# Kernel tuning notes

Hardware: AMD Instinct MI355X
Metric: run time of the kernel (lower is better)

The kernel has to match this reference:

```python
import jax, jax.numpy as jnp
import numpy as np

B, T, S = 2, 1024, 1024
D, H, L = 512, 8, 4
E, K, FF = 8, 2, 2048
V, BLK = 32000, 2048
DH = D // H
EPS = 1e-5


def setup_inputs() -> dict:
    key = jax.random.key(0)
    ks = jax.random.split(key, 20)
    n = lambda k, shp: jax.random.normal(k, shp, dtype=jnp.float32) * 0.02
    return {
        "decoder_input_ids": jax.random.randint(ks[0], (B, T), 0, V, dtype=jnp.int32),
        "enc_out": jax.random.normal(ks[1], (B, S, D), dtype=jnp.float32),
        "attention_mask": jnp.ones((B, T), dtype=jnp.int32),
        "embed_table": n(ks[2], (V, D)),
        "pos_table": n(ks[3], (BLK, D)),
        "sa_w": n(ks[4], (L, 4, D, D)),   # q,k,v,o projections for self-attn
        "sa_b": jnp.zeros((L, 4, D), jnp.float32),
        "ca_w": n(ks[5], (L, 4, D, D)),   # q,k,v,o projections for cross-attn
        "ca_b": jnp.zeros((L, 4, D), jnp.float32),
        "ln_g": jnp.ones((L, 3, D), jnp.float32),
        "ln_b": jnp.zeros((L, 3, D), jnp.float32),
        "router_w": n(ks[6], (L, D, E)),
        "router_b": jnp.zeros((L, E), jnp.float32),
        "exp_w1": n(ks[7], (L, E, D, FF)),
        "exp_b1": jnp.zeros((L, E, FF), jnp.float32),
        "exp_w2": n(ks[8], (L, E, FF, D)),
        "exp_b2": jnp.zeros((L, E, D), jnp.float32),
    }


def _layer_norm(x, g, b):
    mu = jnp.mean(x, axis=-1, keepdims=True)
    var = jnp.mean(jnp.square(x - mu), axis=-1, keepdims=True)
    return (x - mu) * jax.lax.rsqrt(var + EPS) * g + b


def _mha(q_in, kv_in, w, b, mask):
    # w: [4, D, D]; 0=q,1=k,2=v,3=out
    def split_heads(t):
        Bn, Tn, _ = t.shape
        return t.reshape(Bn, Tn, H, DH).transpose(0, 2, 1, 3)  # [B,H,T,dh]
    q = split_heads(q_in @ w[0] + b[0])
    k = split_heads(kv_in @ w[1] + b[1])
    v = split_heads(kv_in @ w[2] + b[2])
    scores = jnp.einsum("bhqd,bhkd->bhqk", q, k) / jnp.sqrt(jnp.float32(DH))
    if mask is not None:
        scores = jnp.where(mask, scores, jnp.float32(-1e9))
    attn = jax.nn.softmax(scores, axis=-1)
    out = jnp.einsum("bhqk,bhkd->bhqd", attn, v)
    out = out.transpose(0, 2, 1, 3).reshape(q_in.shape[0], q_in.shape[1], D)
    return out @ w[3] + b[3]


def _sparse_moe(x, rw, rb, w1, b1, w2, b2):
    # Router: softmax over experts, keep top-k, renormalize kept weights.
    logits = x @ rw + rb                       # [B,T,E]
    probs = jax.nn.softmax(logits, axis=-1)
    topv, topi = jax.lax.top_k(probs, K)       # [B,T,K]
    kmask = jnp.sum(jax.nn.one_hot(topi, E, dtype=x.dtype), axis=-2)  # [B,T,E]
    gates = probs * kmask
    gates = gates / jnp.sum(gates, axis=-1, keepdims=True)
    # Dense expert compute (faithful math, vectorized over experts).
    h = jax.nn.relu(jnp.einsum("btd,edf->btef", x, w1) + b1)   # [B,T,E,FF]
    eo = jnp.einsum("btef,efd->bted", h, w2) + b2              # [B,T,E,D]
    out = jnp.einsum("bte,bted->btd", gates, eo)
    # Load-balancing aux loss: E * sum_e f_e * P_e
    f = jnp.mean(kmask, axis=(0, 1))
    p = jnp.mean(probs, axis=(0, 1))
    lb = jnp.float32(E) * jnp.sum(f * p)
    return out, lb


def reference(decoder_input_ids, enc_out, attention_mask, embed_table, pos_table,
              sa_w, sa_b, ca_w, ca_b, ln_g, ln_b, router_w, router_b,
              exp_w1, exp_b1, exp_w2, exp_b2):
    Bn, Tn = decoder_input_ids.shape
    y = embed_table[decoder_input_ids] + pos_table[:Tn]  # [B,T,D]
    causal = jnp.tril(jnp.ones((Tn, Tn), dtype=bool))
    am = attention_mask.astype(bool)[:, None, None, :]   # [B,1,1,T]
    mask = causal[None, None] & am                       # [B,1,T,T]
    lb_total = jnp.float32(0.0)
    for i in range(L):
        sa = _mha(y, y, sa_w[i], sa_b[i], mask)
        y = _layer_norm(y + sa, ln_g[i, 0], ln_b[i, 0])
        ca = _mha(y, enc_out, ca_w[i], ca_b[i], None)
        y = _layer_norm(y + ca, ln_g[i, 1], ln_b[i, 1])
        mo, lb = _sparse_moe(y, router_w[i], router_b[i], exp_w1[i], exp_b1[i], exp_w2[i], exp_b2[i])
        lb_total = lb_total + lb
        y = _layer_norm(y + mo, ln_g[i, 2], ln_b[i, 2])
    return y, lb_total
```

## Files before the change

### kernel.cpp

```cpp
#include <hip/hip_runtime.h>
#include <math.h>

#define Bb 2
#define Tt 1024
#define Ss 1024
#define Dd 512
#define Hh 8
#define Ll 4
#define Ee 8
#define FFf 2048
#define Mm 2048
#define NPp 4096
#define EPSF 1e-5f
#define DD_ (Dd*Dd)
#define LOSC 1024.0f
#define ILOSC (1.0f/1024.0f)
#define RBLK 64
#define IMm (1.0f/(float)Mm)

typedef _Float16 f16;
typedef __attribute__((ext_vector_type(8))) _Float16 f16x8;
typedef __attribute__((ext_vector_type(4))) _Float16 f16x4;
typedef __attribute__((ext_vector_type(4))) float f32x4;

__device__ __forceinline__ void fsplit(float x, f16& h, f16& l) {
  h = (f16)x;
  l = (f16)((x - (float)h) * LOSC);
}

__device__ __forceinline__ void load16(const void* g, void* l) {
  __builtin_amdgcn_global_load_lds(
      (const __attribute__((address_space(1))) void*)g,
      (__attribute__((address_space(3))) void*)l, 16, 0, 0);
}

__global__ void embed_kernel(const int* __restrict__ ids,
                             const float* __restrict__ emb,
                             const float* __restrict__ pos,
                             float* __restrict__ Y,
                             f16* __restrict__ Yh, f16* __restrict__ Yl) {
  int m = blockIdx.x;
  int t = m % Tt;
  int id = ids[m];
  for (int d = threadIdx.x; d < Dd; d += 256) {
    float v = emb[(size_t)id * Dd + d] + pos[(size_t)t * Dd + d];
    Y[(size_t)m * Dd + d] = v;
    f16 h, l; fsplit(v, h, l);
    Yh[(size_t)m * Dd + d] = h;
    Yl[(size_t)m * Dd + d] = l;
  }
}

__global__ void cvt_split_kernel(const float* __restrict__ src,
                                 f16* __restrict__ dh, f16* __restrict__ dl) {
  size_t i = ((size_t)blockIdx.x * 256 + threadIdx.x) * 4;
  float4 v = *reinterpret_cast<const float4*>(&src[i]);
  float a[4] = {v.x, v.y, v.z, v.w};
#pragma unroll
  for (int j = 0; j < 4; j++) { f16 h, l; fsplit(a[j], h, l); dh[i + j] = h; dl[i + j] = l; }
}

__global__ void zero_kernel(float* __restrict__ p) {
  size_t i = ((size_t)blockIdx.x * 256 + threadIdx.x) * 4;
  *reinterpret_cast<float4*>(&p[i]) = make_float4(0.f, 0.f, 0.f, 0.f);
}

__global__ __launch_bounds__(256)
void transpose_split(const float* __restrict__ src,
                     f16* __restrict__ dstH, f16* __restrict__ dstL,
                     int Kd, int Nd) {
  __shared__ float Tl[32][33];
  size_t zo = (size_t)blockIdx.z * Kd * Nd;
  int k0 = blockIdx.y * 32, n0 = blockIdx.x * 32;
  int t = threadIdx.x;
  int r = t >> 3, c = t & 7;
  float4 v = *reinterpret_cast<const float4*>(&src[zo + (size_t)(k0 + r) * Nd + n0 + c * 4]);
  Tl[r][c * 4 + 0] = v.x; Tl[r][c * 4 + 1] = v.y;
  Tl[r][c * 4 + 2] = v.z; Tl[r][c * 4 + 3] = v.w;
  __syncthreads();
  int nl = t >> 3, kq = t & 7;
  f16x4 hv, lv;
#pragma unroll
  for (int i = 0; i < 4; i++) {
    f16 h, l; fsplit(Tl[kq * 4 + i][nl], h, l);
    hv[i] = h; lv[i] = l;
  }
  size_t o = zo + (size_t)(n0 + nl) * Kd + k0 + kq * 4;
  *reinterpret_cast<f16x4*>(&dstH[o]) = hv;
  *reinterpret_cast<f16x4*>(&dstL[o]) = lv;
}

template <bool GATHER, bool OSPLIT, bool RELU, bool GATE, int KS>
__global__ __launch_bounds__(256)
void mm128(const f16* __restrict__ Ah_, const f16* __restrict__ Al_, int lda,
           const f16* __restrict__ Bh_, const f16* __restrict__ Bl_,
           const float* __restrict__ bias,
           float* __restrict__ Cf, f16* __restrict__ Ch, f16* __restrict__ Cl, int ldc,
           int Mtot, int N, int K,
           const int* __restrict__ tok, const float* __restrict__ gate,
           const int* __restrict__ offs, const int* __restrict__ cnt) {
  __shared__ f16 Ash[128 * 32];
  __shared__ f16 Asl[128 * 32];
  __shared__ f16 Bsh[128 * 32];
  __shared__ f16 Bsl[128 * 32];
  int zz = blockIdx.z;
  int e  = (KS > 1) ? (zz / KS) : zz;
  int ks = (KS > 1) ? (zz % KS) : 0;
  int base = 0, ne = Mtot;
  if (offs) { base = offs[e]; ne = cnt[e]; }
  int m0 = blockIdx.y * 128;
  if (m0 >= ne) return;
  int rem = ne - m0;
  Bh_ += (size_t)e * N * K;
  Bl_ += (size_t)e * N * K;
  bias += (size_t)e * N;

  int t = threadIdx.x;
  int rr = t >> 2, cc = t & 3;
  int csw = cc ^ ((rr >> 1) & 3);
  int gr0 = base + m0 + rr;      if (gr0 > Mtot - 1) gr0 = Mtot - 1;
  int gr1 = base + m0 + rr + 64; if (gr1 > Mtot - 1) gr1 = Mtot - 1;
  int arow0 = GATHER ? tok[gr0] : gr0;
  int arow1 = GATHER ? tok[gr1] : gr1;
  size_t aoff0 = (size_t)arow0 * lda + csw * 8;
  size_t aoff1 = (size_t)arow1 * lda + csw * 8;
  size_t boff0 = (size_t)(blockIdx.x * 128 + rr) * K + csw * 8;
  size_t boff1 = (size_t)(blockIdx.x * 128 + rr + 64) * K + csw * 8;

  int lane = t & 63, wv = t >> 6;
  int quad = lane >> 4, m16 = lane & 15;
  int sw = quad ^ ((m16 >> 1) & 3);
  int wm = (wv >> 1) * 64, wn = (wv & 1) * 64;

  f32x4 accm[4][4], accc[4][4];
#pragma unroll
  for (int i = 0; i < 4; i++)
#pragma unroll
    for (int j = 0; j < 4; j++) {
      accm[i][j] = (f32x4){0.f, 0.f, 0.f, 0.f};
      accc[i][j] = (f32x4){0.f, 0.f, 0.f, 0.f};
    }

  int kper = K / KS;
  int kbeg = ks * kper;
  for (int kc = kbeg; kc < kbeg + kper; kc += 32) {
    load16(Ah_ + aoff0 + kc, &Ash[t * 8]);
    load16(Ah_ + aoff1 + kc, &Ash[2048 + t * 8]);
    load16(Al_ + aoff0 + kc, &Asl[t * 8]);
    load16(Al_ + aoff1 + kc, &Asl[2048 + t * 8]);
    load16(Bh_ + boff0 + kc, &Bsh[t * 8]);
    load16(Bh_ + boff1 + kc, &Bsh[2048 + t * 8]);
    load16(Bl_ + boff0 + kc, &Bsl[t * 8]);
    load16(Bl_ + boff1 + kc, &Bsl[2048 + t * 8]);
    __syncthreads();
    f16x8 ah[4], al[4];
#pragma unroll
    for (int i = 0; i < 4; i++) {
      ah[i] = *reinterpret_cast<const f16x8*>(&Ash[(wm + i * 16 + m16) * 32 + sw * 8]);
      al[i] = *reinterpret_cast<const f16x8*>(&Asl[(wm + i * 16 + m16) * 32 + sw * 8]);
    }
#pragma unroll
    for (int j = 0; j < 4; j++) {
      f16x8 bh = *reinterpret_cast<const f16x8*>(&Bsh[(wn + j * 16 + m16) * 32 + sw * 8]);
      f16x8 bl = *reinterpret_cast<const f16x8*>(&Bsl[(wn + j * 16 + m16) * 32 + sw * 8]);
#pragma unroll
      for (int i = 0; i < 4; i++) {
        accm[i][j] = __builtin_amdgcn_mfma_f32_16x16x32_f16(ah[i], bh, accm[i][j], 0, 0, 0);
        accc[i][j] = __builtin_amdgcn_mfma_f32_16x16x32_f16(ah[i], bl, accc[i][j], 0, 0, 0);
        accc[i][j] = __builtin_amdgcn_mfma_f32_16x16x32_f16(al[i], bh, accc[i][j], 0, 0, 0);
      }
    }
    __syncthreads();
  }

#pragma unroll
  for (int i = 0; i < 4; i++) {
#pragma unroll
    for (int reg = 0; reg < 4; reg++) {
      int lr = wm + i * 16 + quad * 4 + reg;
      if (lr < rem) {
        size_t grow = (size_t)(base + m0 + lr);
        float gv = 1.f;
        if (GATE) gv = gate[grow];
#pragma unroll
        for (int j = 0; j < 4; j++) {
          int col = blockIdx.x * 128 + wn + j * 16 + m16;
          float bv = (KS == 1 || ks == 0) ? bias[col] : 0.f;
          float v = accm[i][j][reg] + accc[i][j][reg] * ILOSC + bv;
          if (RELU) v = fmaxf(v, 0.f);
          if (GATE) v *= gv;
          if (OSPLIT) {
            f16 h, l; fsplit(v, h, l);
            Ch[grow * ldc + col] = h;
            Cl[grow * ldc + col] = l;
          } else if (KS > 1) {
            atomicAdd(&Cf[grow * ldc + col], v);
          } else {
            Cf[grow * ldc + col] = v;
          }
        }
      }
    }
  }
}

__global__ __launch_bounds__(256)
void attn_mfma(const f16* __restrict__ Qh, const f16* __restrict__ Ql, int sq, int oq,
               const f16* __restrict__ Kh, const f16* __restrict__ Kl, int sk, int ok,
               const f16* __restrict__ Vh, const f16* __restrict__ Vl, int sv, int ov,
               f16* __restrict__ Oh, f16* __restrict__ Ol,
               const int* __restrict__ amask, int causal, int nK) {
  __shared__ f16 Ksh[32 * 64];
  __shared__ f16 Ksl[32 * 64];
  __shared__ f16 Vth[64 * 32];
  __shared__ f16 Vtl[64 * 32];
  __shared__ f16 Psh[4 * 16 * 32];
  __shared__ f16 Psl[4 * 16 * 32];

  int bh = blockIdx.x;
  int b = bh >> 3, hd = bh & 7;
  int t = threadIdx.x;
  int wv = t >> 6, lane = t & 63;
  int quad = lane >> 4, m16 = lane & 15;
  int qfrow = blockIdx.y * 64 + wv * 16 + m16;
  int qcbase = blockIdx.y * 64 + wv * 16 + quad * 4;

  size_t qoff = (size_t)(b * Tt + qfrow) * sq + oq + hd * 64;
  f16x8 qh0 = *reinterpret_cast<const f16x8*>(Qh + qoff + quad * 8);
  f16x8 qh1 = *reinterpret_cast<const f16x8*>(Qh + qoff + 32 + quad * 8);
  f16x8 ql0 = *reinterpret_cast<const f16x8*>(Ql + qoff + quad * 8);
  f16x8 ql1 = *reinterpret_cast<const f16x8*>(Ql + qoff + 32 + quad * 8);

  f32x4 Om[4], Oc[4];
#pragma unroll
  for (int c = 0; c < 4; c++) {
    Om[c] = (f32x4){0.f, 0.f, 0.f, 0.f};
    Oc[c] = (f32x4){0.f, 0.f, 0.f, 0.f};
  }
  float mr[4] = {-1e30f, -1e30f, -1e30f, -1e30f};
  float lrw[4] = {0.f, 0.f, 0.f, 0.f};

  int NT = causal ? (blockIdx.y * 2 + 2) : (nK >> 5);
  int myNT = causal ? (((blockIdx.y * 64 + wv * 16 + 15) >> 5) + 1) : NT;

  int rk = t >> 3, gs = t & 7, gsrc = gs ^ (rk & 7);
  int rv = t & 31, gv = t >> 5;

  for (int kt = 0; kt < NT; ++kt) {
    __syncthreads();
    {
      size_t krow = (size_t)(b * 1024 + kt * 32 + rk) * sk + ok + hd * 64 + gsrc * 8;
      *reinterpret_cast<f16x8*>(&Ksh[t * 8]) = *reinterpret_cast<const f16x8*>(Kh + krow);
      *reinterpret_cast<f16x8*>(&Ksl[t * 8]) = *reinterpret_cast<const f16x8*>(Kl + krow);
      size_t vrow = (size_t)(b * 1024 + kt * 32 + rv) * sv + ov + hd * 64 + gv * 8;
      f16x8 vh8 = *reinterpret_cast<const f16x8*>(Vh + vrow);
      f16x8 vl8 = *reinterpret_cast<const f16x8*>(Vl + vrow);
#pragma unroll
      for (int i = 0; i < 8; i++) {
        Vth[(gv * 8 + i) * 32 + rv] = vh8[i];
        Vtl[(gv * 8 + i) * 32 + rv] = vl8[i];
      }
    }
    __syncthreads();

    if (kt < myNT) {
      f32x4 S0m = (f32x4){0.f, 0.f, 0.f, 0.f}, S0c = S0m, S1m = S0m, S1c = S0m;
      {
        int key0 = m16, key1 = 16 + m16;
        int g0a = (quad) ^ (key0 & 7), g0b = (4 + quad) ^ (key0 & 7);
        int g1a = (quad) ^ (key1 & 7), g1b = (4 + quad) ^ (key1 & 7);
        f16x8 kh0a = *reinterpret_cast<const f16x8*>(&Ksh[key0 * 64 + g0a * 8]);
        f16x8 kh0b = *reinterpret_cast<const f16x8*>(&Ksh[key0 * 64 + g0b * 8]);
        f16x8 kl0a = *reinterpret_cast<const f16x8*>(&Ksl[key0 * 64 + g0a * 8]);
        f16x8 kl0b = *reinterpret_cast<const f16x8*>(&Ksl[key0 * 64 + g0b * 8]);
        S0m = __builtin_amdgcn_mfma_f32_16x16x32_f16(qh0, kh0a, S0m, 0, 0, 0);
        S0m = __builtin_amdgcn_mfma_f32_16x16x32_f16(qh1, kh0b, S0m, 0, 0, 0);
        S0c = __builtin_amdgcn_mfma_f32_16x16x32_f16(qh0, kl0a, S0c, 0, 0, 0);
        S0c = __builtin_amdgcn_mfma_f32_16x16x32_f16(qh1, kl0b, S0c, 0, 0, 0);
        S0c = __builtin_amdgcn_mfma_f32_16x16x32_f16(ql0, kh0a, S0c, 0, 0, 0);
        S0c = __builtin_amdgcn_mfma_f32_16x16x32_f16(ql1, kh0b, S0c, 0, 0, 0);
        f16x8 kh1a = *reinterpret_cast<const f16x8*>(&Ksh[key1 * 64 + g1a * 8]);
        f16x8 kh1b = *reinterpret_cast<const f16x8*>(&Ksh[key1 * 64 + g1b * 8]);
        f16x8 kl1a = *reinterpret_cast<const f16x8*>(&Ksl[key1 * 64 + g1a * 8]);
        f16x8 kl1b = *reinterpret_cast<const f16x8*>(&Ksl[key1 * 64 + g1b * 8]);
        S1m = __builtin_amdgcn_mfma_f32_16x16x32_f16(qh0, kh1a, S1m, 0, 0, 0);
        S1m = __builtin_amdgcn_mfma_f32_16x16x32_f16(qh1, kh1b, S1m, 0, 0, 0);
        S1c = __builtin_amdgcn_mfma_f32_16x16x32_f16(qh0, kl1a, S1c, 0, 0, 0);
        S1c = __builtin_amdgcn_mfma_f32_16x16x32_f16(qh1, kl1b, S1c, 0, 0, 0);
        S1c = __builtin_amdgcn_mfma_f32_16x16x32_f16(ql0, kh1a, S1c, 0, 0, 0);
        S1c = __builtin_amdgcn_mfma_f32_16x16x32_f16(ql1, kh1b, S1c, 0, 0, 0);
      }
      float S0[4], S1[4];
      int key0 = kt * 32 + m16, key1 = kt * 32 + 16 + m16;
      int am0 = amask ? amask[b * nK + key0] : 1;
      int am1 = amask ? amask[b * nK + key1] : 1;
#pragma unroll
      for (int reg = 0; reg < 4; reg++) {
        int qr = qcbase + reg;
        bool ok0 = am0 && (!causal || key0 <= qr);
        bool ok1 = am1 && (!causal || key1 <= qr);
        S0[reg] = ok0 ? (S0m[reg] + S0c[reg] * ILOSC) * 0.125f : -1e9f;
        S1[reg] = ok1 ? (S1m[reg] + S1c[reg] * ILOSC) * 0.125f : -1e9f;
      }
      float mt[4], al4[4], rs[4];
#pragma unroll
      for (int reg = 0; reg < 4; reg++) mt[reg] = fmaxf(S0[reg], S1[reg]);
#pragma unroll
      for (int off = 1; off < 16; off <<= 1)
#pragma unroll
        for (int reg = 0; reg < 4; reg++) mt[reg] = fmaxf(mt[reg], __shfl_xor(mt[reg], off, 64));
#pragma unroll
      for (int reg = 0; reg < 4; reg++) {
        float mn = fmaxf(mr[reg], mt[reg]);
        al4[reg] = expf(mr[reg] - mn);
        mr[reg] = mn;
        S0[reg] = expf(S0[reg] - mn);
        S1[reg] = expf(S1[reg] - mn);
        rs[reg] = S0[reg] + S1[reg];
      }
#pragma unroll
      for (int off = 1; off < 16; off <<= 1)
#pragma unroll
        for (int reg = 0; reg < 4; reg++) rs[reg] += __shfl_xor(rs[reg], off, 64);
#pragma unroll
      for (int reg = 0; reg < 4; reg++) {
        lrw[reg] = lrw[reg] * al4[reg] + rs[reg];
#pragma unroll
        for (int c = 0; c < 4; c++) { Om[c][reg] *= al4[reg]; Oc[c][reg] *= al4[reg]; }
        int prow = wv * 16 + quad * 4 + reg;
        f16 ph, pl;
        fsplit(S0[reg], ph, pl);
        Psh[prow * 32 + m16] = ph; Psl[prow * 32 + m16] = pl;
        fsplit(S1[reg], ph, pl);
        Psh[prow * 32 + 16 + m16] = ph; Psl[prow * 32 + 16 + m16] = pl;
      }
      __builtin_amdgcn_sched_barrier(0);
      f16x8 pah = *reinterpret_cast<const f16x8*>(&Psh[(wv * 16 + m16) * 32 + quad * 8]);
      f16x8 pal = *reinterpret_cast<const f16x8*>(&Psl[(wv * 16 + m16) * 32 + quad * 8]);
#pragma unroll
      for (int c = 0; c < 4; c++) {
        f16x8 vbh = *reinterpret_cast<const f16x8*>(&Vth[(c * 16 + m16) * 32 + quad * 8]);
        f16x8 vbl = *reinterpret_cast<const f16x8*>(&Vtl[(c * 16 + m16) * 32 + quad * 8]);
        Om[c] = __builtin_amdgcn_mfma_f32_16x16x32_f16(pah, vbh, Om[c], 0, 0, 0);
        Oc[c] = __builtin_amdgcn_mfma_f32_16x16x32_f16(pah, vbl, Oc[c], 0, 0, 0);
        Oc[c] = __builtin_amdgcn_mfma_f32_16x16x32_f16(pal, vbh, Oc[c], 0, 0, 0);
      }
    }
  }
#pragma unroll
  for (int reg = 0; reg < 4; reg++) {
    int qr = qcbase + reg;
    float inv = 1.f / lrw[reg];
#pragma unroll
    for (int c = 0; c < 4; c++) {
      float o = (Om[c][reg] + Oc[c][reg] * ILOSC) * inv;
      f16 hh, ll; fsplit(o, hh, ll);
      size_t oo = (size_t)(b * Tt + qr) * Dd + hd * 64 + c * 16 + m16;
      Oh[oo] = hh;
      Ol[oo] = ll;
    }
  }
}

__global__ __launch_bounds__(256)
void add_ln_kernel(float* __restrict__ Y, f16* __restrict__ Yh, f16* __restrict__ Yl,
                   const float* __restrict__ Aadd,
                   const float* __restrict__ g, const float* __restrict__ bb) {
  int tid = threadIdx.x;
  size_t base = (size_t)blockIdx.x * Dd;
  __shared__ float red[256];
  __shared__ float mu_s, rs_s;
  float x0 = Y[base + tid] + Aadd[base + tid];
  float x1 = Y[base + 256 + tid] + Aadd[base + 256 + tid];
  red[tid] = x0 + x1; __syncthreads();
  for (int s2 = 128; s2 > 0; s2 >>= 1) { if (tid < s2) red[tid] += red[tid + s2]; __syncthreads(); }
  if (tid == 0) mu_s = red[0] / (float)Dd;
  __syncthreads();
  float mu = mu_s;
  float d0 = x0 - mu, d1 = x1 - mu;
  red[tid] = d0 * d0 + d1 * d1; __syncthreads();
  for (int s2 = 128; s2 > 0; s2 >>= 1) { if (tid < s2) red[tid] += red[tid + s2]; __syncthreads(); }
  if (tid == 0) rs_s = rsqrtf(red[0] / (float)Dd + EPSF);
  __syncthreads();
  float rs = rs_s;
  float o0 = d0 * rs * g[tid] + bb[tid];
  float o1 = d1 * rs * g[256 + tid] + bb[256 + tid];
  f16 h, l;
  Y[base + tid] = o0; fsplit(o0, h, l); Yh[base + tid] = h; Yl[base + tid] = l;
  Y[base + 256 + tid] = o1; fsplit(o1, h, l); Yh[base + 256 + tid] = h; Yl[base + 256 + tid] = l;
}

__global__ __launch_bounds__(256)
void combine_ln_kernel(float* __restrict__ Y, f16* __restrict__ Yh, f16* __restrict__ Yl,
                       const float* __restrict__ pout, const int* __restrict__ slot,
                       const float* __restrict__ g, const float* __restrict__ bb) {
  int tid = threadIdx.x;
  int m = blockIdx.x;
  size_t base = (size_t)m * Dd;
  int s0 = slot[m * 2 + 0], s1 = slot[m * 2 + 1];
  __shared__ float red[256];
  __shared__ float mu_s, rs_s;
  float x0 = Y[base + tid] + pout[(size_t)s0 * Dd + tid] + pout[(size_t)s1 * Dd + tid];
  float x1 = Y[base + 256 + tid] + pout[(size_t)s0 * Dd + 256 + tid] + pout[(size_t)s1 * Dd + 256 + tid];
  red[tid] = x0 + x1; __syncthreads();
  for (int s2 = 128; s2 > 0; s2 >>= 1) { if (tid < s2) red[tid] += red[tid + s2]; __syncthreads(); }
  if (tid == 0) mu_s = red[0] / (float)Dd;
  __syncthreads();
  float mu = mu_s;
  float d0 = x0 - mu, d1 = x1 - mu;
  red[tid] = d0 * d0 + d1 * d1; __syncthreads();
  for (int s2 = 128; s2 > 0; s2 >>= 1) { if (tid < s2) red[tid] += red[tid + s2]; __syncthreads(); }
  if (tid == 0) rs_s = rsqrtf(red[0] / (float)Dd + EPSF);
  __syncthreads();
  float rs = rs_s;
  float o0 = d0 * rs * g[tid] + bb[tid];
  float o1 = d1 * rs * g[256 + tid] + bb[256 + tid];
  f16 h, l;
  Y[base + tid] = o0; fsplit(o0, h, l); Yh[base + tid] = h; Yl[base + tid] = l;
  Y[base + 256 + tid] = o1; fsplit(o1, h, l); Yh[base + 256 + tid] = h; Yl[base + 256 + tid] = l;
}

__global__ __launch_bounds__(256)
void router_kernel(const float* __restrict__ Y, const float* __restrict__ rw,
                   const float* __restrict__ rb, float* __restrict__ gates,
                   int* __restrict__ topi, int* __restrict__ part_cnt,
                   float* __restrict__ part_sumP) {
  int wv = threadIdx.x >> 6, lane = threadIdx.x & 63;
  __shared__ float wsum[4][Ee];
  __shared__ int wcnt[4][Ee];
  float w[8][Ee];
#pragma unroll
  for (int dd = 0; dd < 8; dd++) {
    const float4* rp = reinterpret_cast<const float4*>(&rw[(size_t)(dd * 64 + lane) * Ee]);
    float4 a = rp[0], b4 = rp[1];
    w[dd][0] = a.x; w[dd][1] = a.y; w[dd][2] = a.z; w[dd][3] = a.w;
    w[dd][4] = b4.x; w[dd][5] = b4.y; w[dd][6] = b4.z; w[dd][7] = b4.w;
  }
  float rbv[Ee];
#pragma unroll
  for (int e = 0; e < Ee; e++) rbv[e] = rb[e];

  float psum[Ee]; int pcnt[Ee];
#pragma unroll
  for (int e = 0; e < Ee; e++) { psum[e] = 0.f; pcnt[e] = 0; }

  int m0 = blockIdx.x * 32 + wv * 8;
  for (int j = 0; j < 8; j++) {
    int m = m0 + j;
    const float* yr = Y + (size_t)m * Dd;
    float yv[8];
#pragma unroll
    for (int dd = 0; dd < 8; dd++) yv[dd] = yr[dd * 64 + lane];
    float acc[Ee];
#pragma unroll
    for (int e = 0; e < Ee; e++) acc[e] = 0.f;
#pragma unroll
    for (int dd = 0; dd < 8; dd++)
#pragma unroll
      for (int e = 0; e < Ee; e++) acc[e] += yv[dd] * w[dd][e];
#pragma unroll
    for (int off = 32; off; off >>= 1)
#pragma unroll
      for (int e = 0; e < Ee; e++) acc[e] += __shfl_xor(acc[e], off, 64);
    if (lane == 0) {
      float pv[Ee];
      float mx = -1e30f;
#pragma unroll
      for (int e = 0; e < Ee; e++) { pv[e] = acc[e] + rbv[e]; mx = fmaxf(mx, pv[e]); }
      float ssum = 0.f;
#pragma unroll
      for (int e = 0; e < Ee; e++) { pv[e] = expf(pv[e] - mx); ssum += pv[e]; }
      float invs = 1.f / ssum;
#pragma unroll
      for (int e = 0; e < Ee; e++) { pv[e] *= invs; psum[e] += pv[e]; }
      int i1 = 0;
#pragma unroll
      for (int e = 1; e < Ee; e++) if (pv[e] > pv[i1]) i1 = e;
      int i2 = (i1 == 0) ? 1 : 0;
#pragma unroll
      for (int e = 0; e < Ee; e++) if (e != i1 && pv[e] > pv[i2]) i2 = e;
      float gs = pv[i1] + pv[i2];
      gates[m * 2 + 0] = pv[i1] / gs;
      gates[m * 2 + 1] = pv[i2] / gs;
      topi[m * 2 + 0] = i1;
      topi[m * 2 + 1] = i2;
#pragma unroll
      for (int e = 0; e < Ee; e++) pcnt[e] += (e == i1) + (e == i2);
    }
  }
  if (lane == 0) {
#pragma unroll
    for (int e = 0; e < Ee; e++) { wsum[wv][e] = psum[e]; wcnt[wv][e] = pcnt[e]; }
  }
  __syncthreads();
  if (threadIdx.x < Ee) {
    int e = threadIdx.x;
    float s = wsum[0][e] + wsum[1][e] + wsum[2][e] + wsum[3][e];
    int c = wcnt[0][e] + wcnt[1][e] + wcnt[2][e] + wcnt[3][e];
    part_sumP[blockIdx.x * Ee + e] = s;
    part_cnt[blockIdx.x * Ee + e] = c;
  }
}

__global__ void prefix_lb_kernel(const int* __restrict__ part_cnt,
                                 const float* __restrict__ part_sumP,
                                 int* __restrict__ cnt, int* __restrict__ offs,
                                 int* __restrict__ fill, float* __restrict__ lb_acc) {
  __shared__ int sc[Ee];
  __shared__ float ss[Ee];
  int t = threadIdx.x;
  if (t < Ee) {
    int c = 0; float s = 0.f;
    for (int b2 = 0; b2 < RBLK; b2++) { c += part_cnt[b2 * Ee + t]; s += part_sumP[b2 * Ee + t]; }
    sc[t] = c; ss[t] = s;
    cnt[t] = c; fill[t] = 0;
  }
  __syncthreads();
  if (t == 0) {
    int run = 0;
    float lb = 0.f;
    for (int e = 0; e < Ee; e++) {
      offs[e] = run; run += sc[e];
      lb += ((float)sc[e] * IMm) * (ss[e] * IMm);
    }
    *lb_acc += (float)Ee * lb;
  }
}

__global__ __launch_bounds__(256)
void scatter_kernel(const int* __restrict__ topi, const float* __restrict__ gates,
                    const int* __restrict__ offs, int* __restrict__ fill,
                    int* __restrict__ pair_tok, float* __restrict__ pair_gate,
                    int* __restrict__ slot) {
  __shared__ int lcnt[Ee];
  __shared__ int lbase[Ee];
  int t = threadIdx.x;
  int m = blockIdx.x * 256 + t;
  if (t < Ee) lcnt[t] = 0;
  __syncthreads();
  int e0 = topi[m * 2 + 0], e1 = topi[m * 2 + 1];
  float g0 = gates[m * 2 + 0], g1 = gates[m * 2 + 1];
  int p0 = atomicAdd(&lcnt[e0], 1);
  int p1 = atomicAdd(&lcnt[e1], 1);
  __syncthreads();
  if (t < Ee) lbase[t] = atomicAdd(&fill[t], lcnt[t]);
  __syncthreads();
  int i0 = offs[e0] + lbase[e0] + p0;
  int i1 = offs[e1] + lbase[e1] + p1;
  pair_tok[i0] = m; pair_gate[i0] = g0; slot[m * 2 + 0] = i0;
  pair_tok[i1] = m; pair_gate[i1] = g1; slot[m * 2 + 1] = i1;
}

__global__ void init_lb_kernel(float* lb_acc) {
  if (threadIdx.x == 0) *lb_acc = 0.f;
}

__global__ void finalize_kernel(const float* __restrict__ Y,
                                const float* __restrict__ lb_acc,
                                float* __restrict__ out) {
  size_t i = (size_t)blockIdx.x * 256 + threadIdx.x;
  const size_t n = (size_t)Mm * Dd;
  if (i < n) out[i] = Y[i];
  if (i == 0) out[n] = *lb_acc;
}

extern "C" void kernel_launch(void* const* d_in, const int* in_sizes, int n_in,
                              void* d_out, int out_size, void* d_ws, size_t ws_size,
                              hipStream_t stream) {
  const int*   ids   = (const int*)d_in[0];
  const float* enc   = (const float*)d_in[1];
  const int*   amask = (const int*)d_in[2];
  const float* emb   = (const float*)d_in[3];
  const float* pos   = (const float*)d_in[4];
  const float* sa_w  = (const float*)d_in[5];
  const float* sa_b  = (const float*)d_in[6];
  const float* ca_w  = (const float*)d_in[7];
  const float* ca_b  = (const float*)d_in[8];
  const float* ln_g  = (const float*)d_in[9];
  const float* ln_b  = (const float*)d_in[10];
  const float* rw    = (const float*)d_in[11];
  const float* rb    = (const float*)d_in[12];
  const float* ew1   = (const float*)d_in[13];
  const float* eb1   = (const float*)d_in[14];
  const float* ew2   = (const float*)d_in[15];
  const float* eb2   = (const float*)d_in[16];
  float* out = (float*)d_out;

  char* p = (char*)d_ws;
  auto alloc = [&](size_t bytes) { void* r = p; p += (bytes + 255) & ~(size_t)255; return r; };
  float* y    = (float*)alloc((size_t)Mm * Dd * 4);
  float* proj = (float*)alloc((size_t)Mm * Dd * 4);
  float* pout = (float*)alloc((size_t)NPp * Dd * 4);
  f16* yh   = (f16*)alloc((size_t)Mm * Dd * 2);
  f16* yl   = (f16*)alloc((size_t)Mm * Dd * 2);
  f16* ench = (f16*)alloc((size_t)Mm * Dd * 2);
  f16* encl = (f16*)alloc((size_t)Mm * Dd * 2);
  f16* qkvh = (f16*)alloc((size_t)Mm * 1536 * 2);
  f16* qkvl = (f16*)alloc((size_t)Mm * 1536 * 2);
  f16* qch  = (f16*)alloc((size_t)Mm * Dd * 2);
  f16* qcl  = (f16*)alloc((size_t)Mm * Dd * 2);
  f16* atth = (f16*)alloc((size_t)Mm * Dd * 2);
  f16* attl = (f16*)alloc((size_t)Mm * Dd * 2);
  f16* ckvh = (f16*)alloc((size_t)Mm * 1024 * 2);
  f16* ckvl = (f16*)alloc((size_t)Mm * 1024 * 2);
  f16* moeh = (f16*)alloc((size_t)NPp * FFf * 2);
  f16* moel = (f16*)alloc((size_t)NPp * FFf * 2);
  f16* saTh = (f16*)alloc((size_t)Ll * 4 * DD_ * 2);
  f16* saTl = (f16*)alloc((size_t)Ll * 4 * DD_ * 2);
  f16* caTh = (f16*)alloc((size_t)Ll * 4 * DD_ * 2);
  f16* caTl = (f16*)alloc((size_t)Ll * 4 * DD_ * 2);
  f16* w1Th = (f16*)alloc((size_t)Ee * Dd * FFf * 2);
  f16* w1Tl = (f16*)alloc((size_t)Ee * Dd * FFf * 2);
  f16* w2Th = (f16*)alloc((size_t)Ee * Dd * FFf * 2);
  f16* w2Tl = (f16*)alloc((size_t)Ee * Dd * FFf * 2);
  float* gates     = (float*)alloc((size_t)Mm * 2 * 4);
  float* pair_gate = (float*)alloc((size_t)NPp * 4);
  float* part_sumP = (float*)alloc((size_t)RBLK * Ee * 4);
  float* lb_acc    = (float*)alloc(4);
  int* topi     = (int*)alloc((size_t)Mm * 2 * 4);
  int* pair_tok = (int*)alloc((size_t)NPp * 4);
  int* slot     = (int*)alloc((size_t)Mm * 2 * 4);
  int* part_cnt = (int*)alloc((size_t)RBLK * Ee * 4);
  int* cnt      = (int*)alloc(Ee * 4);
  int* offs     = (int*)alloc(Ee * 4);
  int* fill     = (int*)alloc(Ee * 4);

  init_lb_kernel<<<1, 64, 0, stream>>>(lb_acc);
  embed_kernel<<<Mm, 256, 0, stream>>>(ids, emb, pos, y, yh, yl);
  cvt_split_kernel<<<(Mm * Dd) / 1024, 256, 0, stream>>>(enc, ench, encl);
  transpose_split<<<dim3(16, 16, 16), 256, 0, stream>>>(sa_w, saTh, saTl, Dd, Dd);
  transpose_split<<<dim3(16, 16, 16), 256, 0, stream>>>(ca_w, caTh, caTl, Dd, Dd);

  dim3 gAttn(Bb * Hh, Tt / 64);

  for (int i = 0; i < Ll; i++) {
    transpose_split<<<dim3(64, 16, 8), 256, 0, stream>>>(ew1 + (size_t)i * Ee * Dd * FFf, w1Th, w1Tl, Dd, FFf);
    transpose_split<<<dim3(16, 64, 8), 256, 0, stream>>>(ew2 + (size_t)i * Ee * FFf * Dd, w2Th, w2Tl, FFf, Dd);

    const f16* saThl = saTh + (size_t)i * 4 * DD_;
    const f16* saTll = saTl + (size_t)i * 4 * DD_;
    const f16* caThl = caTh + (size_t)i * 4 * DD_;
    const f16* caTll = caTl + (size_t)i * 4 * DD_;
    const float* sabl = sa_b + (size_t)i * 4 * Dd;
    const float* cabl = ca_b + (size_t)i * 4 * Dd;

    mm128<false, true, false, false, 1><<<dim3(8, 16, 1), 256, 0, stream>>>(
        ench, encl, Dd, caThl + DD_, caTll + DD_, cabl + Dd,
        nullptr, ckvh, ckvl, 1024, Mm, 1024, Dd, nullptr, nullptr, nullptr, nullptr);
    mm128<false, true, false, false, 1><<<dim3(12, 16, 1), 256, 0, stream>>>(
        yh, yl, Dd, saThl, saTll, sabl,
        nullptr, qkvh, qkvl, 1536, Mm, 1536, Dd, nullptr, nullptr, nullptr, nullptr);
    attn_mfma<<<gAttn, 256, 0, stream>>>(qkvh, qkvl, 1536, 0, qkvh, qkvl, 1536, 512,
                                         qkvh, qkvl, 1536, 1024, atth, attl, amask, 1, Tt);
    mm128<false, false, false, false, 1><<<dim3(4, 16, 1), 256, 0, stream>>>(
        atth, attl, Dd, saThl + 3 * DD_, saTll + 3 * DD_, sabl + 3 * Dd,
        proj, nullptr, nullptr, Dd, Mm, Dd, Dd, nullptr, nullptr, nullptr, nullptr);
    add_ln_kernel<<<Mm, 256, 0, stream>>>(y, yh, yl, proj,
                                          ln_g + (size_t)(i * 3 + 0) * Dd, ln_b + (size_t)(i * 3 + 0) * Dd);
    mm128<false, true, false, false, 1><<<dim3(4, 16, 1), 256, 0, stream>>>(
        yh, yl, Dd, caThl, caTll, cabl,
        nullptr, qch, qcl, Dd, Mm, Dd, Dd, nullptr, nullptr, nullptr, nullptr);
    attn_mfma<<<gAttn, 256, 0, stream>>>(qch, qcl, Dd, 0, ckvh, ckvl, 1024, 0,
                                         ckvh, ckvl, 1024, 512, atth, attl, nullptr, 0, Ss);
    mm128<false, false, false, false, 1><<<dim3(4, 16, 1), 256, 0, stream>>>(
        atth, attl, Dd, caThl + 3 * DD_, caTll + 3 * DD_, cabl + 3 * Dd,
        proj, nullptr, nullptr, Dd, Mm, Dd, Dd, nullptr, nullptr, nullptr, nullptr);
    add_ln_kernel<<<Mm, 256, 0, stream>>>(y, yh, yl, proj,
                                          ln_g + (size_t)(i * 3 + 1) * Dd, ln_b + (size_t)(i * 3 + 1) * Dd);
    router_kernel<<<RBLK, 256, 0, stream>>>(y, rw + (size_t)i * Dd * Ee, rb + (size_t)i * Ee,
                                            gates, topi, part_cnt, part_sumP);
    prefix_lb_kernel<<<1, 64, 0, stream>>>(part_cnt, part_sumP, cnt, offs, lb_acc ? fill : fill, lb_acc);
    scatter_kernel<<<Mm / 256, 256, 0, stream>>>(topi, gates, offs, fill, pair_tok, pair_gate, slot);
    zero_kernel<<<((size_t)NPp * Dd) / 1024, 256, 0, stream>>>(pout);
    mm128<true, true, true, false, 1><<<dim3(16, 32, 8), 256, 0, stream>>>(
        yh, yl, Dd, w1Th, w1Tl, eb1 + (size_t)i * Ee * FFf,
        nullptr, moeh, moel, FFf, NPp, FFf, Dd, pair_tok, nullptr, offs, cnt);
    mm128<false, false, false, true, 4><<<dim3(4, 32, Ee * 4), 256, 0, stream>>>(
        moeh, moel, FFf, w2Th, w2Tl, eb2 + (size_t)i * Ee * Dd,
        pout, nullptr, nullptr, Dd, NPp, Dd, FFf, nullptr, pair_gate, offs, cnt);
    combine_ln_kernel<<<Mm, 256, 0, stream>>>(y, yh, yl, pout, slot,
                                              ln_g + (size_t)(i * 3 + 2) * Dd, ln_b + (size_t)(i * 3 + 2) * Dd);
  }

  finalize_kernel<<<(int)(((size_t)Mm * Dd + 256) / 256) + 1, 256, 0, stream>>>(y, lb_acc, out);
}
```

Baseline: 2.873 ms.

## Double-buffer GEMM shared tiles and replace atomic split-K with per-split buffers

The mm128 GEMM now uses double-buffered LDS tiles. The next K-chunk's global-to-shared loads are issued before the MFMA work on the current chunk, with an explicit vmcnt wait and barrier at the end of each step. The expert second GEMM drops from split-K 4 with atomicAdd into a zeroed buffer to split-K 2, where each split writes its own output plane. The combine kernel sums both planes, which removes the zero kernel and the atomics. In exchange, LDS use doubles (which may lower occupancy), there is less K-parallelism in the down-projection, and the pout buffer is twice as large.

```diff
diff --git a/kernel.cpp b/kernel.cpp
--- a/kernel.cpp
+++ b/kernel.cpp
@@ -60,11 +60,6 @@
   for (int j = 0; j < 4; j++) { f16 h, l; fsplit(a[j], h, l); dh[i + j] = h; dl[i + j] = l; }
 }
 
-__global__ void zero_kernel(float* __restrict__ p) {
-  size_t i = ((size_t)blockIdx.x * 256 + threadIdx.x) * 4;
-  *reinterpret_cast<float4*>(&p[i]) = make_float4(0.f, 0.f, 0.f, 0.f);
-}
-
 __global__ __launch_bounds__(256)
 void transpose_split(const float* __restrict__ src,
                      f16* __restrict__ dstH, f16* __restrict__ dstL,
@@ -99,10 +94,10 @@
            int Mtot, int N, int K,
            const int* __restrict__ tok, const float* __restrict__ gate,
            const int* __restrict__ offs, const int* __restrict__ cnt) {
-  __shared__ f16 Ash[128 * 32];
-  __shared__ f16 Asl[128 * 32];
-  __shared__ f16 Bsh[128 * 32];
-  __shared__ f16 Bsl[128 * 32];
+  __shared__ f16 Ash[2][128 * 32];
+  __shared__ f16 Asl[2][128 * 32];
+  __shared__ f16 Bsh[2][128 * 32];
+  __shared__ f16 Bsl[2][128 * 32];
   int zz = blockIdx.z;
   int e  = (KS > 1) ? (zz / KS) : zz;
   int ks = (KS > 1) ? (zz % KS) : 0;
@@ -114,6 +109,7 @@
   Bh_ += (size_t)e * N * K;
   Bl_ += (size_t)e * N * K;
   bias += (size_t)e * N;
+  if (KS > 1) Cf += (size_t)ks * (size_t)Mtot * (size_t)ldc;
 
   int t = threadIdx.x;
   int rr = t >> 2, cc = t & 3;
@@ -143,26 +139,36 @@
 
   int kper = K / KS;
   int kbeg = ks * kper;
-  for (int kc = kbeg; kc < kbeg + kper; kc += 32) {
-    load16(Ah_ + aoff0 + kc, &Ash[t * 8]);
-    load16(Ah_ + aoff1 + kc, &Ash[2048 + t * 8]);
-    load16(Al_ + aoff0 + kc, &Asl[t * 8]);
-    load16(Al_ + aoff1 + kc, &Asl[2048 + t * 8]);
-    load16(Bh_ + boff0 + kc, &Bsh[t * 8]);
-    load16(Bh_ + boff1 + kc, &Bsh[2048 + t * 8]);
-    load16(Bl_ + boff0 + kc, &Bsl[t * 8]);
-    load16(Bl_ + boff1 + kc, &Bsl[2048 + t * 8]);
-    __syncthreads();
+  int nt = kper >> 5;
+
+  auto STAGE = [&](int bf, int kc) {
+    load16(Ah_ + aoff0 + kc, &Ash[bf][t * 8]);
+    load16(Ah_ + aoff1 + kc, &Ash[bf][2048 + t * 8]);
+    load16(Al_ + aoff0 + kc, &Asl[bf][t * 8]);
+    load16(Al_ + aoff1 + kc, &Asl[bf][2048 + t * 8]);
+    load16(Bh_ + boff0 + kc, &Bsh[bf][t * 8]);
+    load16(Bh_ + boff1 + kc, &Bsh[bf][2048 + t * 8]);
+    load16(Bl_ + boff0 + kc, &Bsl[bf][t * 8]);
+    load16(Bl_ + boff1 + kc, &Bsl[bf][2048 + t * 8]);
+  };
+
+  STAGE(0, kbeg);
+  asm volatile("s_waitcnt vmcnt(0)" ::: "memory");
+  __builtin_amdgcn_s_barrier();
+
+  for (int tt = 0; tt < nt; ++tt) {
+    int bf = tt & 1;
+    if (tt + 1 < nt) STAGE(bf ^ 1, kbeg + (tt + 1) * 32);
     f16x8 ah[4], al[4];
 #pragma unroll
     for (int i = 0; i < 4; i++) {
-      ah[i] = *reinterpret_cast<const f16x8*>(&Ash[(wm + i * 16 + m16) * 32 + sw * 8]);
-      al[i] = *reinterpret_cast<const f16x8*>(&Asl[(wm + i * 16 + m16) * 32 + sw * 8]);
+      ah[i] = *reinterpret_cast<const f16x8*>(&Ash[bf][(wm + i * 16 + m16) * 32 + sw * 8]);
+      al[i] = *reinterpret_cast<const f16x8*>(&Asl[bf][(wm + i * 16 + m16) * 32 + sw * 8]);
     }
 #pragma unroll
     for (int j = 0; j < 4; j++) {
-      f16x8 bh = *reinterpret_cast<const f16x8*>(&Bsh[(wn + j * 16 + m16) * 32 + sw * 8]);
-      f16x8 bl = *reinterpret_cast<const f16x8*>(&Bsl[(wn + j * 16 + m16) * 32 + sw * 8]);
+      f16x8 bh = *reinterpret_cast<const f16x8*>(&Bsh[bf][(wn + j * 16 + m16) * 32 + sw * 8]);
+      f16x8 bl = *reinterpret_cast<const f16x8*>(&Bsl[bf][(wn + j * 16 + m16) * 32 + sw * 8]);
 #pragma unroll
       for (int i = 0; i < 4; i++) {
         accm[i][j] = __builtin_amdgcn_mfma_f32_16x16x32_f16(ah[i], bh, accm[i][j], 0, 0, 0);
@@ -170,7 +176,8 @@
         accc[i][j] = __builtin_amdgcn_mfma_f32_16x16x32_f16(al[i], bh, accc[i][j], 0, 0, 0);
       }
     }
-    __syncthreads();
+    asm volatile("s_waitcnt vmcnt(0)" ::: "memory");
+    __builtin_amdgcn_s_barrier();
   }
 
 #pragma unroll
@@ -193,8 +200,6 @@
             f16 h, l; fsplit(v, h, l);
             Ch[grow * ldc + col] = h;
             Cl[grow * ldc + col] = l;
-          } else if (KS > 1) {
-            atomicAdd(&Cf[grow * ldc + col], v);
           } else {
             Cf[grow * ldc + col] = v;
           }
@@ -392,7 +397,8 @@
 
 __global__ __launch_bounds__(256)
 void combine_ln_kernel(float* __restrict__ Y, f16* __restrict__ Yh, f16* __restrict__ Yl,
-                       const float* __restrict__ pout, const int* __restrict__ slot,
+                       const float* __restrict__ pout, const float* __restrict__ pout2,
+                       const int* __restrict__ slot,
                        const float* __restrict__ g, const float* __restrict__ bb) {
   int tid = threadIdx.x;
   int m = blockIdx.x;
@@ -400,8 +406,10 @@
   int s0 = slot[m * 2 + 0], s1 = slot[m * 2 + 1];
   __shared__ float red[256];
   __shared__ float mu_s, rs_s;
-  float x0 = Y[base + tid] + pout[(size_t)s0 * Dd + tid] + pout[(size_t)s1 * Dd + tid];
-  float x1 = Y[base + 256 + tid] + pout[(size_t)s0 * Dd + 256 + tid] + pout[(size_t)s1 * Dd + 256 + tid];
+  float x0 = Y[base + tid] + pout[(size_t)s0 * Dd + tid] + pout[(size_t)s1 * Dd + tid]
+           + pout2[(size_t)s0 * Dd + tid] + pout2[(size_t)s1 * Dd + tid];
+  float x1 = Y[base + 256 + tid] + pout[(size_t)s0 * Dd + 256 + tid] + pout[(size_t)s1 * Dd + 256 + tid]
+           + pout2[(size_t)s0 * Dd + 256 + tid] + pout2[(size_t)s1 * Dd + 256 + tid];
   red[tid] = x0 + x1; __syncthreads();
   for (int s2 = 128; s2 > 0; s2 >>= 1) { if (tid < s2) red[tid] += red[tid + s2]; __syncthreads(); }
   if (tid == 0) mu_s = red[0] / (float)Dd;
@@ -590,7 +598,7 @@
   auto alloc = [&](size_t bytes) { void* r = p; p += (bytes + 255) & ~(size_t)255; return r; };
   float* y    = (float*)alloc((size_t)Mm * Dd * 4);
   float* proj = (float*)alloc((size_t)Mm * Dd * 4);
-  float* pout = (float*)alloc((size_t)NPp * Dd * 4);
+  float* pout = (float*)alloc((size_t)2 * NPp * Dd * 4);
   f16* yh   = (f16*)alloc((size_t)Mm * Dd * 2);
   f16* yl   = (f16*)alloc((size_t)Mm * Dd * 2);
   f16* ench = (f16*)alloc((size_t)Mm * Dd * 2);
@@ -624,6 +632,7 @@
   int* cnt      = (int*)alloc(Ee * 4);
   int* offs     = (int*)alloc(Ee * 4);
   int* fill     = (int*)alloc(Ee * 4);
+  float* pout2 = pout + (size_t)NPp * Dd;
 
   init_lb_kernel<<<1, 64, 0, stream>>>(lb_acc);
   embed_kernel<<<Mm, 256, 0, stream>>>(ids, emb, pos, y, yh, yl);
@@ -669,16 +678,15 @@
                                           ln_g + (size_t)(i * 3 + 1) * Dd, ln_b + (size_t)(i * 3 + 1) * Dd);
     router_kernel<<<RBLK, 256, 0, stream>>>(y, rw + (size_t)i * Dd * Ee, rb + (size_t)i * Ee,
                                             gates, topi, part_cnt, part_sumP);
-    prefix_lb_kernel<<<1, 64, 0, stream>>>(part_cnt, part_sumP, cnt, offs, lb_acc ? fill : fill, lb_acc);
+    prefix_lb_kernel<<<1, 64, 0, stream>>>(part_cnt, part_sumP, cnt, offs, fill, lb_acc);
     scatter_kernel<<<Mm / 256, 256, 0, stream>>>(topi, gates, offs, fill, pair_tok, pair_gate, slot);
-    zero_kernel<<<((size_t)NPp * Dd) / 1024, 256, 0, stream>>>(pout);
     mm128<true, true, true, false, 1><<<dim3(16, 32, 8), 256, 0, stream>>>(
         yh, yl, Dd, w1Th, w1Tl, eb1 + (size_t)i * Ee * FFf,
         nullptr, moeh, moel, FFf, NPp, FFf, Dd, pair_tok, nullptr, offs, cnt);
-    mm128<false, false, false, true, 4><<<dim3(4, 32, Ee * 4), 256, 0, stream>>>(
+    mm128<false, false, false, true, 2><<<dim3(4, 32, Ee * 2), 256, 0, stream>>>(
         moeh, moel, FFf, w2Th, w2Tl, eb2 + (size_t)i * Ee * Dd,
         pout, nullptr, nullptr, Dd, NPp, Dd, FFf, nullptr, pair_gate, offs, cnt);
-    combine_ln_kernel<<<Mm, 256, 0, stream>>>(y, yh, yl, pout, slot,
+    combine_ln_kernel<<<Mm, 256, 0, stream>>>(y, yh, yl, pout, pout2, slot,
                                               ln_g + (size_t)(i * 3 + 2) * Dd, ln_b + (size_t)(i * 3 + 2) * Dd);
   }
 
```

New measurement: 2.437 ms. 1.18x faster.
